# Kernel tuning notes

Measured on AMD Instinct MI355X. Metric: run time of the kernel, lower is better.

The kernel has to match this reference:

```python
import jax, jax.numpy as jnp
import numpy as np

HEADS = 16
DIM_HEAD = 64
SCALE = DIM_HEAD ** -0.5


def shift(x):
    # Transformer-XL relative shift trick. x: [..., i, j] -> [..., i, j]
    *pre, i, j = x.shape
    x = jnp.concatenate([x, jnp.zeros((*pre, i, i), x.dtype)], axis=-1)
    l = i + j - 1
    x = x.reshape(*pre, -1)
    pad = (-x.shape[-1]) % l
    x = jnp.concatenate([x, jnp.zeros((*pre, pad), x.dtype)], axis=-1)
    x = x.reshape(*pre, -1, l)
    return x[..., :i, i - 1:]


def setup_inputs() -> dict:
    key = jax.random.key(0)
    ks = jax.random.split(key, 8)
    b, t, e = 2, 1024, 1024
    mem_len, lmem_len = 1024, 128
    kv_len = t + mem_len + lmem_len
    return {
        "x": jax.random.normal(ks[0], (b, t, e), jnp.float32),
        "mem": jax.random.normal(ks[1], (b, mem_len, e), jnp.float32),
        "lmem": jax.random.normal(ks[2], (b, lmem_len, e), jnp.float32),
        "pos_emb": jax.random.normal(ks[3], (HEADS, kv_len, DIM_HEAD), jnp.float32),
        "input_mask": jnp.ones((b, t), bool),
        "Wq": jax.random.normal(ks[4], (e, e), jnp.float32) * 0.02,
        "Wkv": jax.random.normal(ks[5], (e, 2 * e), jnp.float32) * 0.02,
        "Wout": jax.random.normal(ks[6], (e, e), jnp.float32) * 0.02,
        "bout": jnp.zeros((e,), jnp.float32),
    }


def reference(x, mem, lmem, pos_emb, input_mask, Wq, Wkv, Wout, bout):
    b, t, e = x.shape
    h, dh = HEADS, DIM_HEAD
    mem_len, lmem_len = mem.shape[1], lmem.shape[1]
    total_mem = mem_len + lmem_len

    q = x @ Wq
    kv_input = jnp.concatenate([lmem, mem, x], axis=1)  # [b, kv_len, e]
    kv_len = kv_input.shape[1]
    k, v = jnp.split(kv_input @ Wkv, 2, axis=-1)

    def merge_heads(z):
        return z.reshape(b, -1, h, dh).transpose(0, 2, 1, 3)  # [b, h, n, dh]

    q, k, v = merge_heads(q), merge_heads(k), merge_heads(v)

    dots = jnp.einsum('bhid,bhjd->bhij', q, k) * SCALE  # [b, h, t, kv_len]

    pe = pos_emb[:, -kv_len:].astype(q.dtype)
    pos_dots = jnp.einsum('bhid,hjd->bhij', q, pe) * SCALE
    dots = dots + shift(pos_dots)

    mask_value = -jnp.finfo(dots.dtype).max

    pad_mask = input_mask[:, None, :, None] & input_mask[:, None, None, :]
    pad_mask = jnp.pad(pad_mask, ((0, 0), (0, 0), (0, 0), (total_mem, 0)), constant_values=True)
    dots = jnp.where(pad_mask, dots, mask_value)

    causal = jnp.triu(jnp.ones((t, t + total_mem), bool), k=1 + total_mem)
    dots = jnp.where(causal[None, None], mask_value, dots)

    attn = jax.nn.softmax(dots, axis=-1)
    out = jnp.einsum('bhij,bhjd->bhid', attn, v)
    out = out.transpose(0, 2, 1, 3).reshape(b, t, -1)
    return out @ Wout + bout
```

## Files before the change

kernel.cpp:

```cpp
#include <hip/hip_runtime.h>


typedef unsigned int   u32;
typedef unsigned short u16;
typedef unsigned long long u64;
typedef __attribute__((ext_vector_type(8))) short short8;
typedef __attribute__((ext_vector_type(4))) float f32x4;
typedef __attribute__((ext_vector_type(4))) u32   u32x4;

#define DEVI static __device__ __forceinline__
#define MFMA_BF16 __builtin_amdgcn_mfma_f32_16x16x32_bf16

DEVI u16 f2bf(float f) {
  u32 u = __builtin_bit_cast(u32, f);
  return (u16)((u + 0x7FFFu + ((u >> 16) & 1u)) >> 16);
}
DEVI float bf2f(u16 h) { u32 u = (u32)h << 16; return __builtin_bit_cast(float, u); }
DEVI u32 pk2(float lo, float hi) { return (u32)f2bf(lo) | ((u32)f2bf(hi) << 16); }
DEVI u32 cvtpk(float lo, float hi) {
  u32 r;
  asm("v_cvt_pk_bf16_f32 %0, %1, %2" : "=v"(r) : "v"(lo), "v"(hi));
  return r;
}

constexpr int T_ = 1024, E_ = 1024, KV = 2176, H_ = 16;
constexpr float QSCALE = 0.125f * 1.44269504088896f;

__global__ void k_prep_all(const float* __restrict__ x, const float* __restrict__ mem,
                           const float* __restrict__ lmem, const float* __restrict__ pos,
                           const float* __restrict__ Wq, const float* __restrict__ Wkv,
                           const float* __restrict__ Wout,
                           u16* __restrict__ kvin, u16* __restrict__ pe,
                           u16* __restrict__ WallT, u16* __restrict__ WoT) {
  __shared__ float tile[32][33];
  int bid = blockIdx.x, t = threadIdx.x;
  if (bid < 3264) {
    if (bid < 2176) {
      int u = bid * 256 + t;
      int b = u / (KV * E_ / 8);
      int r = u % (KV * E_ / 8);
      int j = r >> 7;
      int e8 = (r & 127) << 3;
      const float* src;
      if (j < 128)        src = lmem + ((size_t)(b * 128 + j) * E_ + e8);
      else if (j < 1152)  src = mem  + ((size_t)(b * 1024 + (j - 128)) * E_ + e8);
      else                src = x    + ((size_t)(b * 1024 + (j - 1152)) * E_ + e8);
      float4 a = ((const float4*)src)[0];
      float4 c = ((const float4*)src)[1];
      u32x4 o = { pk2(a.x, a.y), pk2(a.z, a.w), pk2(c.x, c.y), pk2(c.z, c.w) };
      *(u32x4*)(kvin + (size_t)u * 8) = o;
    } else {
      size_t u = (size_t)(bid - 2176) * 256 + t;
      float4 a = ((const float4*)(pos + u * 8))[0];
      float4 c = ((const float4*)(pos + u * 8))[1];
      u32x4 o = { pk2(a.x, a.y), pk2(a.z, a.w), pk2(c.x, c.y), pk2(c.z, c.w) };
      *(u32x4*)(pe + u * 8) = o;
    }
    return;
  }
  const float* src; u16* dst; int K, N, n0, k0;
  if (bid < 4288)      { int r = bid - 3264; src = Wq;   dst = WallT;             K = 1024; N = 1024; n0 = (r & 31) * 32; k0 = (r >> 5) * 32; }
  else if (bid < 6336) { int r = bid - 4288; src = Wkv;  dst = WallT + 1024*1024; K = 1024; N = 2048; n0 = (r & 63) * 32; k0 = (r >> 6) * 32; }
  else                 { int r = bid - 6336; src = Wout; dst = WoT;               K = 1024; N = 1024; n0 = (r & 31) * 32; k0 = (r >> 5) * 32; }
  int tx = t & 31, ty = t >> 5;
#pragma unroll
  for (int s = 0; s < 4; s++) tile[ty + 8 * s][tx] = src[(size_t)(k0 + ty + 8 * s) * N + n0 + tx];
  __syncthreads();
#pragma unroll
  for (int s = 0; s < 4; s++)
    dst[(size_t)(n0 + ty + 8 * s) * K + k0 + tx] = f2bf(tile[tx][ty + 8 * s]);
}

__global__ __launch_bounds__(256, 3)
void k_gemm_qkv(const u16* __restrict__ kvin, const u16* __restrict__ WallT,
                u16* __restrict__ qb, u16* __restrict__ kb, u16* __restrict__ vtb) {
  int bid = blockIdx.x;
  int b = bid / 336;
  int r = bid % 336;
  int nt, mt;
  if (r < 64) { nt = r >> 3; mt = 9 + (r & 7); }
  else { r -= 64; nt = 8 + r / 17; mt = r % 17; }

  const u16* A  = kvin + ((size_t)b * KV + (size_t)mt * 128) * E_;
  const u16* Bm = WallT + (size_t)nt * 128 * E_;

  __shared__ u16 As[2][128 * 40];
  __shared__ u16 Bs[2][128 * 40];

  int t = threadIdx.x;
  int wid = t >> 6, lane = t & 63;
  int wr = wid >> 1, wc = wid & 1;
  int l15 = lane & 15, l4 = lane >> 4;

  f32x4 acc[4][4] = {};
  int arow = t >> 2, aslot = t & 3;

  u32x4 ra[2], rb[2];
  auto ld = [&](int kt_) {
    int k0 = kt_ * 32;
#pragma unroll
    for (int p = 0; p < 2; p++) {
      ra[p] = *(const u32x4*)(A  + (size_t)(arow + 64 * p) * E_ + k0 + aslot * 8);
      rb[p] = *(const u32x4*)(Bm + (size_t)(arow + 64 * p) * E_ + k0 + aslot * 8);
    }
  };
  auto st = [&](int buf) {
#pragma unroll
    for (int p = 0; p < 2; p++) {
      *(u32x4*)(As[buf] + (arow + 64 * p) * 40 + aslot * 8) = ra[p];
      *(u32x4*)(Bs[buf] + (arow + 64 * p) * 40 + aslot * 8) = rb[p];
    }
  };

  ld(0); st(0); ld(1);
  for (int kt = 0; kt < 32; kt++) {
    __syncthreads();
    int buf = kt & 1;
    short8 af[4], bfv[4];
#pragma unroll
    for (int m = 0; m < 4; m++)
      af[m] = *(const short8*)(As[buf] + (wr * 64 + m * 16 + l15) * 40 + l4 * 8);
#pragma unroll
    for (int n = 0; n < 4; n++)
      bfv[n] = *(const short8*)(Bs[buf] + (wc * 64 + n * 16 + l15) * 40 + l4 * 8);
#pragma unroll
    for (int m = 0; m < 4; m++)
#pragma unroll
      for (int n = 0; n < 4; n++)
        acc[m][n] = MFMA_BF16(af[m], bfv[n], acc[m][n], 0, 0, 0);
    if (kt + 1 < 32) st(buf ^ 1);
    if (kt + 2 < 32) ld(kt + 2);
  }
  int grow_base = mt * 128 + wr * 64;
  int ncol_base = nt * 128 + wc * 64;
  if (nt < 8) {
#pragma unroll
    for (int m = 0; m < 4; m++)
#pragma unroll
      for (int n = 0; n < 4; n++) {
        int col = ncol_base + n * 16 + l15;
        int head = col >> 6, d = col & 63;
#pragma unroll
        for (int rg = 0; rg < 4; rg++) {
          int row = grow_base + m * 16 + l4 * 4 + rg - 1152;
          qb[(((size_t)b * 16 + head) * 1024 + row) * 64 + d] = f2bf(acc[m][n][rg] * QSCALE);
        }
      }
  } else if (nt < 16) {
#pragma unroll
    for (int m = 0; m < 4; m++)
#pragma unroll
      for (int n = 0; n < 4; n++) {
        int c = ncol_base + n * 16 + l15 - 1024;
        int head = c >> 6, d = c & 63;
#pragma unroll
        for (int rg = 0; rg < 4; rg++) {
          int row = grow_base + m * 16 + l4 * 4 + rg;
          kb[(((size_t)b * 16 + head) * KV + row) * 64 + d] = f2bf(acc[m][n][rg]);
        }
      }
  } else {
#pragma unroll
    for (int m = 0; m < 4; m++)
#pragma unroll
      for (int n = 0; n < 4; n++) {
        int c = ncol_base + n * 16 + l15 - 2048;
        int head = c >> 6, d = c & 63;
        int jb = grow_base + m * 16 + l4 * 4;
        u64 pv = (u64)f2bf(acc[m][n][0]) | ((u64)f2bf(acc[m][n][1]) << 16)
               | ((u64)f2bf(acc[m][n][2]) << 32) | ((u64)f2bf(acc[m][n][3]) << 48);
        *(u64*)(vtb + (((size_t)b * 16 + head) * 64 + d) * KV + jb) = pv;
      }
  }
}

__global__ __launch_bounds__(256, 2)
void k_attn(const u16* __restrict__ qb, const u16* __restrict__ kb,
            const u16* __restrict__ vtb, const u16* __restrict__ peb,
            u16* __restrict__ ao) {
  int bid = blockIdx.x;
  int xcd = bid & 7;
  int itr = (bid >> 3) & 15;
  int g   = bid >> 7;
  int it  = (g >= 2) ? (15 - itr) : itr;
  int bh = g * 8 + xcd;
  int b = bh >> 4, h = bh & 15;
  int i0 = it * 64;

  __shared__ u16 Klds[2][64][72];
  __shared__ u16 Vt[2][64][72];
  __shared__ u16 Band[64][136];
  __shared__ u16 Pb[4][16][72];

  int t = threadIdx.x, wid = t >> 6, lane = t & 63;
  int l15 = lane & 15, l4 = lane >> 4;
  int il = wid * 16 + l15;
  int srow = t >> 3, ssl = t & 7;

  const u16* kbase  = kb  + (size_t)bh * KV * 64;
  const u16* vtbase = vtb + (size_t)bh * 64 * KV;
  const u16* pebase = peb + (size_t)h * KV * 64;

  const u16* qptr = qb + ((size_t)bh * 1024 + i0 + il) * 64 + l4 * 8;
  short8 qf0 = *(const short8*)qptr;
  short8 qf1 = *(const short8*)(qptr + 32);

  f32x4 Of[4] = {};
  float mr = -1e30f, lr = 0.f;
  int njt = it + 19;

  u32x4 rk0, rk1, rv0, rv1;
  auto load_regs = [&](int jt_) {
    int j0_ = jt_ * 64;
    rk0 = *(const u32x4*)(kbase + (size_t)(j0_ + srow) * 64 + ssl * 8);
    rk1 = *(const u32x4*)(kbase + (size_t)(j0_ + srow + 32) * 64 + ssl * 8);
    rv0 = *(const u32x4*)(vtbase + (size_t)srow * KV + j0_ + ssl * 8);
    rv1 = *(const u32x4*)(vtbase + (size_t)(srow + 32) * KV + j0_ + ssl * 8);
  };
  auto store_tile = [&](int buf) {
    *(u32x4*)(&Klds[buf][srow][ssl * 8]) = rk0;
    *(u32x4*)(&Klds[buf][srow + 32][ssl * 8]) = rk1;
    *(u32x4*)(&Vt[buf][srow][ssl * 8]) = rv0;
    *(u32x4*)(&Vt[buf][srow + 32][ssl * 8]) = rv1;
  };
  auto load_pe = [&](int prb, short8* pf) {
#pragma unroll
    for (int rc = 0; rc < 4; rc++) {
      int rr = prb + rc * 16 + l15;
#pragma unroll
      for (int kk = 0; kk < 2; kk++)
        pf[rc * 2 + kk] = *(const short8*)(pebase + (size_t)rr * 64 + kk * 32 + l4 * 8);
    }
  };
  auto band_mfma_store = [&](int prb, const short8* pf) {
    f32x4 acc[4];
    __builtin_amdgcn_s_setprio(1);
#pragma unroll
    for (int rc = 0; rc < 4; rc++) {
      f32x4 a = {};
      a = MFMA_BF16(pf[rc * 2 + 0], qf0, a, 0, 0, 0);
      a = MFMA_BF16(pf[rc * 2 + 1], qf1, a, 0, 0, 0);
      acc[rc] = a;
    }
    __builtin_amdgcn_s_setprio(0);
#pragma unroll
    for (int rc = 0; rc < 4; rc++) {
      int rb = prb + rc * 16 + l4 * 4 + il + 1;
      u32 w01 = cvtpk(acc[rc][0], acc[rc][1]);
      u32 w23 = cvtpk(acc[rc][2], acc[rc][3]);
      Band[il][rb & 127]       = (u16)w01;
      Band[il][(rb + 1) & 127] = (u16)(w01 >> 16);
      Band[il][(rb + 2) & 127] = (u16)w23;
      Band[il][(rb + 3) & 127] = (u16)(w23 >> 16);
    }
  };
  auto band_ninf = [&](int prb) {
#pragma unroll
    for (int rc = 0; rc < 4; rc++) {
      int rb = prb + rc * 16 + l4 * 4 + il + 1;
#pragma unroll
      for (int rg = 0; rg < 4; rg++)
        Band[il][(rb + rg) & 127] = 0xFF80u;
    }
  };

  load_regs(0);
  store_tile(0);
  short8 pf[8];
  load_pe(960 - i0, pf);
  band_mfma_store(960 - i0, pf);
  load_pe(1024 - i0, pf);
  load_regs(1);

  int cur = 0;
  for (int jt = 0; jt < njt; jt++) {
    __syncthreads();

    f32x4 sc[4];
    __builtin_amdgcn_s_setprio(1);
#pragma unroll
    for (int jc = 0; jc < 4; jc++) {
      f32x4 a = {};
      short8 k0 = *(const short8*)(&Klds[cur][jc * 16 + l15][l4 * 8]);
      short8 k1 = *(const short8*)(&Klds[cur][jc * 16 + l15][32 + l4 * 8]);
      a = MFMA_BF16(k0, qf0, a, 0, 0, 0);
      a = MFMA_BF16(k1, qf1, a, 0, 0, 0);
      sc[jc] = a;
    }
    __builtin_amdgcn_s_setprio(0);

    if (jt == njt - 1) band_ninf(1024 + 64 * jt - i0);
    else               band_mfma_store(1024 + 64 * jt - i0, pf);
    if (jt + 2 < njt) load_pe(1024 + 64 * (jt + 1) - i0, pf);

    asm volatile("s_waitcnt lgkmcnt(0)" ::: "memory");
    __builtin_amdgcn_sched_barrier(0);

    float P[4][4];
    float mx = -1e30f;
    int cb0 = ((jt - it) & 1) << 6;
#pragma unroll
    for (int jc = 0; jc < 4; jc++) {
      u64 bl = *(const u64*)(&Band[il][cb0 + jc * 16 + l4 * 4]);
#pragma unroll
      for (int rg = 0; rg < 4; rg++) {
        float v = sc[jc][rg] + bf2f((u16)(bl >> (16 * rg)));
        P[jc][rg] = v;
        mx = fmaxf(mx, v);
      }
    }
    if (jt == 0) {
      mx = fmaxf(mx, __shfl_xor(mx, 16, 64));
      mx = fmaxf(mx, __shfl_xor(mx, 32, 64));
      mr = mx;
    }

    float ps = 0.f;
#pragma unroll
    for (int jc = 0; jc < 4; jc++) {
#pragma unroll
      for (int rg = 0; rg < 4; rg++) {
        float p = exp2f(P[jc][rg] - mr);
        P[jc][rg] = p;
        ps += p;
      }
      int cb = jc * 16 + l4 * 4;
      *(u32*)(&Pb[wid][l15][cb])     = cvtpk(P[jc][0], P[jc][1]);
      *(u32*)(&Pb[wid][l15][cb + 2]) = cvtpk(P[jc][2], P[jc][3]);
    }
    short8 vf[8];
#pragma unroll
    for (int df = 0; df < 4; df++)
#pragma unroll
      for (int kk = 0; kk < 2; kk++)
        vf[df * 2 + kk] = *(const short8*)(&Vt[cur][df * 16 + l15][kk * 32 + l4 * 8]);

    if (jt != 0) {
      mx = fmaxf(mx, __shfl_xor(mx, 16, 64));
      mx = fmaxf(mx, __shfl_xor(mx, 32, 64));
    }
    ps += __shfl_xor(ps, 16, 64);
    ps += __shfl_xor(ps, 32, 64);

    asm volatile("s_waitcnt lgkmcnt(0)" ::: "memory");
    __builtin_amdgcn_sched_barrier(0);

    short8 pB0 = *(const short8*)(&Pb[wid][l15][l4 * 8]);
    short8 pB1 = *(const short8*)(&Pb[wid][l15][32 + l4 * 8]);
    __builtin_amdgcn_s_setprio(1);
#pragma unroll
    for (int df = 0; df < 4; df++) {
      Of[df] = MFMA_BF16(vf[df * 2 + 0], pB0, Of[df], 0, 0, 0);
      Of[df] = MFMA_BF16(vf[df * 2 + 1], pB1, Of[df], 0, 0, 0);
    }
    __builtin_amdgcn_s_setprio(0);

    if (jt != 0 && !__all(mx <= mr + 8.0f)) {
      float mnew = fmaxf(mr, mx);
      float fac = exp2f(mr - mnew);
      mr = mnew;
      lr = (lr + ps) * fac;
#pragma unroll
      for (int df = 0; df < 4; df++) Of[df] *= fac;
    } else {
      lr += ps;
    }

    if (jt + 1 < njt) {
      store_tile(cur ^ 1);
      if (jt + 2 < njt) load_regs(jt + 2);
    }
    cur ^= 1;
  }

  float inv = 1.0f / lr;
  size_t ob = ((size_t)b * 1024 + i0 + il) * 1024 + h * 64;
#pragma unroll
  for (int df = 0; df < 4; df++) {
    u64 pv = (u64)f2bf(Of[df][0] * inv)         | ((u64)f2bf(Of[df][1] * inv) << 16)
           | ((u64)f2bf(Of[df][2] * inv) << 32) | ((u64)f2bf(Of[df][3] * inv) << 48);
    *(u64*)(ao + ob + df * 16 + l4 * 4) = pv;
  }
}

__global__ __launch_bounds__(256, 2)
void k_gemm_out(const u16* __restrict__ ao, const u16* __restrict__ WoT,
                const float* __restrict__ bias, float* __restrict__ out) {
  int mt = blockIdx.x & 31, nt = blockIdx.x >> 5;
  const u16* A  = ao  + (size_t)mt * 64 * E_;
  const u16* Bm = WoT + (size_t)nt * 128 * E_;
  __shared__ u16 As[2][64 * 40];
  __shared__ u16 Bs[2][128 * 40];
  int t = threadIdx.x, wid = t >> 6, lane = t & 63;
  int wr = wid >> 1, wc = wid & 1, l15 = lane & 15, l4 = lane >> 4;
  f32x4 acc[2][4] = {};
  int arow = t >> 2, aslot = t & 3;

  u32x4 ra, rb[2];
  auto ld = [&](int kt_) {
    int k0 = kt_ * 32;
    ra = *(const u32x4*)(A + (size_t)arow * E_ + k0 + aslot * 8);
#pragma unroll
    for (int p = 0; p < 2; p++)
      rb[p] = *(const u32x4*)(Bm + (size_t)(arow + 64 * p) * E_ + k0 + aslot * 8);
  };
  auto st = [&](int buf) {
    *(u32x4*)(As[buf] + arow * 40 + aslot * 8) = ra;
#pragma unroll
    for (int p = 0; p < 2; p++)
      *(u32x4*)(Bs[buf] + (arow + 64 * p) * 40 + aslot * 8) = rb[p];
  };

  ld(0); st(0); ld(1);
  for (int kt = 0; kt < 32; kt++) {
    __syncthreads();
    int buf = kt & 1;
    short8 af[2], bfv[4];
#pragma unroll
    for (int m = 0; m < 2; m++)
      af[m] = *(const short8*)(As[buf] + (wr * 32 + m * 16 + l15) * 40 + l4 * 8);
#pragma unroll
    for (int n = 0; n < 4; n++)
      bfv[n] = *(const short8*)(Bs[buf] + (wc * 64 + n * 16 + l15) * 40 + l4 * 8);
#pragma unroll
    for (int m = 0; m < 2; m++)
#pragma unroll
      for (int n = 0; n < 4; n++)
        acc[m][n] = MFMA_BF16(af[m], bfv[n], acc[m][n], 0, 0, 0);
    if (kt + 1 < 32) st(buf ^ 1);
    if (kt + 2 < 32) ld(kt + 2);
  }
#pragma unroll
  for (int n = 0; n < 4; n++) {
    int col = nt * 128 + wc * 64 + n * 16 + l15;
    float bv = bias[col];
#pragma unroll
    for (int m = 0; m < 2; m++) {
      int row = mt * 64 + wr * 32 + m * 16 + l4 * 4;
#pragma unroll
      for (int rg = 0; rg < 4; rg++)
        out[(size_t)(row + rg) * E_ + col] = acc[m][n][rg] + bv;
    }
  }
}

extern "C" void kernel_launch(void* const* d_in, const int* in_sizes, int n_in,
                              void* d_out, int out_size, void* d_ws, size_t ws_size,
                              hipStream_t stream) {
  (void)in_sizes; (void)n_in; (void)out_size; (void)ws_size;
  const float* x    = (const float*)d_in[0];
  const float* mem  = (const float*)d_in[1];
  const float* lmem = (const float*)d_in[2];
  const float* pos  = (const float*)d_in[3];
  const float* Wq   = (const float*)d_in[5];
  const float* Wkv  = (const float*)d_in[6];
  const float* Wout = (const float*)d_in[7];
  const float* bout = (const float*)d_in[8];
  float* out = (float*)d_out;

  u16* kvin  = (u16*)d_ws;
  u16* pe    = kvin  + (size_t)2 * KV * E_;
  u16* WallT = pe    + (size_t)H_ * KV * 64;
  u16* WoT   = WallT + (size_t)3072 * E_;
  u16* qb    = WoT   + (size_t)E_ * E_;
  u16* kb    = qb    + (size_t)2 * H_ * T_ * 64;
  u16* vtb   = kb    + (size_t)2 * H_ * KV * 64;
  u16* ao    = vtb   + (size_t)2 * H_ * KV * 64;

  k_prep_all<<<7360, 256, 0, stream>>>(x, mem, lmem, pos, Wq, Wkv, Wout,
                                       kvin, pe, WallT, WoT);
  k_gemm_qkv<<<672, 256, 0, stream>>>(kvin, WallT, qb, kb, vtb);
  k_attn<<<512, 256, 0, stream>>>(qb, kb, vtb, pe, ao);
  k_gemm_out<<<256, 256, 0, stream>>>(ao, WoT, bout, out);
}
```

Before: 132.2 us.

## Stage QKV GEMM tiles with direct global-to-LDS loads and reorder attention PV MFMA

The QKV projection GEMM now copies A and B tiles from global memory straight into LDS with global_load_lds, in place of loading into registers and then storing to LDS. The LDS rows lose their padding (stride 40 to 32) to match the direct-load layout, and the next tile is issued right after the barrier, giving single-stage prefetch in place of the previous two-deep register prefetch. Unpadded rows may cause LDS bank conflicts on the fragment reads. In the attention loop, the P·V MFMAs are moved ahead of the cross-lane max/sum shuffles so the shuffles can overlap matrix work.

```diff
diff --git a/kernel.cpp b/kernel.cpp
--- a/kernel.cpp
+++ b/kernel.cpp
@@ -21,6 +21,11 @@
   u32 r;
   asm("v_cvt_pk_bf16_f32 %0, %1, %2" : "=v"(r) : "v"(lo), "v"(hi));
   return r;
+}
+DEVI void gll16(const u16* g, u16* l) {
+  __builtin_amdgcn_global_load_lds(
+      (const __attribute__((address_space(1))) u32*)g,
+      (__attribute__((address_space(3))) u32*)l, 16, 0, 0);
 }
 
 constexpr int T_ = 1024, E_ = 1024, KV = 2176, H_ = 16;
@@ -84,8 +89,8 @@
   const u16* A  = kvin + ((size_t)b * KV + (size_t)mt * 128) * E_;
   const u16* Bm = WallT + (size_t)nt * 128 * E_;
 
-  __shared__ u16 As[2][128 * 40];
-  __shared__ u16 Bs[2][128 * 40];
+  __shared__ u16 As[2][128 * 32];
+  __shared__ u16 Bs[2][128 * 32];
 
   int t = threadIdx.x;
   int wid = t >> 6, lane = t & 63;
@@ -93,43 +98,38 @@
   int l15 = lane & 15, l4 = lane >> 4;
 
   f32x4 acc[4][4] = {};
-  int arow = t >> 2, aslot = t & 3;
-
-  u32x4 ra[2], rb[2];
-  auto ld = [&](int kt_) {
+
+  int srowg = wid * 32 + (lane >> 2);
+  int scol  = (lane & 3) * 8;
+  auto stage = [&](int buf, int kt_) {
     int k0 = kt_ * 32;
-#pragma unroll
-    for (int p = 0; p < 2; p++) {
-      ra[p] = *(const u32x4*)(A  + (size_t)(arow + 64 * p) * E_ + k0 + aslot * 8);
-      rb[p] = *(const u32x4*)(Bm + (size_t)(arow + 64 * p) * E_ + k0 + aslot * 8);
-    }
-  };
-  auto st = [&](int buf) {
-#pragma unroll
-    for (int p = 0; p < 2; p++) {
-      *(u32x4*)(As[buf] + (arow + 64 * p) * 40 + aslot * 8) = ra[p];
-      *(u32x4*)(Bs[buf] + (arow + 64 * p) * 40 + aslot * 8) = rb[p];
-    }
-  };
-
-  ld(0); st(0); ld(1);
+    const u16* Ag = A  + (size_t)srowg * E_ + k0 + scol;
+    const u16* Bg = Bm + (size_t)srowg * E_ + k0 + scol;
+    u16* la = As[buf] + wid * 32 * 32;
+    u16* lb = Bs[buf] + wid * 32 * 32;
+    gll16(Ag, la);
+    gll16(Ag + (size_t)16 * E_, la + 16 * 32);
+    gll16(Bg, lb);
+    gll16(Bg + (size_t)16 * E_, lb + 16 * 32);
+  };
+
+  stage(0, 0);
   for (int kt = 0; kt < 32; kt++) {
     __syncthreads();
     int buf = kt & 1;
+    if (kt + 1 < 32) stage(buf ^ 1, kt + 1);
     short8 af[4], bfv[4];
 #pragma unroll
     for (int m = 0; m < 4; m++)
-      af[m] = *(const short8*)(As[buf] + (wr * 64 + m * 16 + l15) * 40 + l4 * 8);
+      af[m] = *(const short8*)(As[buf] + (wr * 64 + m * 16 + l15) * 32 + l4 * 8);
 #pragma unroll
     for (int n = 0; n < 4; n++)
-      bfv[n] = *(const short8*)(Bs[buf] + (wc * 64 + n * 16 + l15) * 40 + l4 * 8);
+      bfv[n] = *(const short8*)(Bs[buf] + (wc * 64 + n * 16 + l15) * 32 + l4 * 8);
 #pragma unroll
     for (int m = 0; m < 4; m++)
 #pragma unroll
       for (int n = 0; n < 4; n++)
         acc[m][n] = MFMA_BF16(af[m], bfv[n], acc[m][n], 0, 0, 0);
-    if (kt + 1 < 32) st(buf ^ 1);
-    if (kt + 2 < 32) ld(kt + 2);
   }
   int grow_base = mt * 128 + wr * 64;
   int ncol_base = nt * 128 + wc * 64;
@@ -335,25 +335,25 @@
       for (int kk = 0; kk < 2; kk++)
         vf[df * 2 + kk] = *(const short8*)(&Vt[cur][df * 16 + l15][kk * 32 + l4 * 8]);
 
+    asm volatile("s_waitcnt lgkmcnt(0)" ::: "memory");
+    __builtin_amdgcn_sched_barrier(0);
+
+    short8 pB0 = *(const short8*)(&Pb[wid][l15][l4 * 8]);
+    short8 pB1 = *(const short8*)(&Pb[wid][l15][32 + l4 * 8]);
+    __builtin_amdgcn_s_setprio(1);
+#pragma unroll
+    for (int df = 0; df < 4; df++) {
+      Of[df] = MFMA_BF16(vf[df * 2 + 0], pB0, Of[df], 0, 0, 0);
+      Of[df] = MFMA_BF16(vf[df * 2 + 1], pB1, Of[df], 0, 0, 0);
+    }
+    __builtin_amdgcn_s_setprio(0);
+
     if (jt != 0) {
       mx = fmaxf(mx, __shfl_xor(mx, 16, 64));
       mx = fmaxf(mx, __shfl_xor(mx, 32, 64));
     }
     ps += __shfl_xor(ps, 16, 64);
     ps += __shfl_xor(ps, 32, 64);
-
-    asm volatile("s_waitcnt lgkmcnt(0)" ::: "memory");
-    __builtin_amdgcn_sched_barrier(0);
-
-    short8 pB0 = *(const short8*)(&Pb[wid][l15][l4 * 8]);
-    short8 pB1 = *(const short8*)(&Pb[wid][l15][32 + l4 * 8]);
-    __builtin_amdgcn_s_setprio(1);
-#pragma unroll
-    for (int df = 0; df < 4; df++) {
-      Of[df] = MFMA_BF16(vf[df * 2 + 0], pB0, Of[df], 0, 0, 0);
-      Of[df] = MFMA_BF16(vf[df * 2 + 1], pB1, Of[df], 0, 0, 0);
-    }
-    __builtin_amdgcn_s_setprio(0);
 
     if (jt != 0 && !__all(mx <= mr + 8.0f)) {
       float mnew = fmaxf(mr, mx);
```

Result: faster. 128.7 us (-2.7%).
